# Optimization experiments

Hardware: AMD Instinct MI355X
Metric: run time of the kernel (lower is better)

## Reference

```python
import jax, jax.numpy as jnp
import numpy as np

N, E, H, XD, ED, YD, L = 10000, 640000, 128, 8, 8, 112, 4
EPS_MSG = 1e-7   # GENConv message eps
EPS_SM = 1e-16   # pyg softmax denom eps
EPS_LN = 1e-5    # layernorm eps


def node_ln(x, g, b):
    # torch.nn.LayerNorm over last dim
    m = x.mean(axis=-1, keepdims=True)
    v = x.var(axis=-1, keepdims=True)
    return (x - m) * jax.lax.rsqrt(v + EPS_LN) * g + b


def graph_ln(x, g, b):
    # pyg LayerNorm mode='graph' (no batch): global mean/std over all nodes+channels
    xc = x - x.mean()
    std = jnp.sqrt((xc * xc).mean())
    return xc / (std + EPS_LN) * g + b


def setup_inputs() -> dict:
    key = jax.random.key(0)
    ks = jax.random.split(key, 10)
    rn = lambda k, s, sc: jax.random.normal(k, s, jnp.float32) * sc
    return {
        "x": jax.random.normal(ks[0], (N, XD), jnp.float32),
        "edge_index": jax.random.randint(ks[1], (2, E), 0, N),
        "edge_attr": jax.random.normal(ks[2], (E, ED), jnp.float32),
        "Wn": rn(ks[3], (XD, H), 0.3), "bn": jnp.zeros((H,), jnp.float32),
        "We": rn(ks[4], (ED, H), 0.3), "be": jnp.zeros((H,), jnp.float32),
        "t": jnp.ones((L,), jnp.float32),
        "W1": rn(ks[5], (L, H, 2 * H), 0.08), "b1": jnp.zeros((L, 2 * H), jnp.float32),
        "g1": jnp.ones((L, 2 * H), jnp.float32), "bt1": jnp.zeros((L, 2 * H), jnp.float32),
        "W2": rn(ks[6], (L, 2 * H, H), 0.08), "b2": jnp.zeros((L, H), jnp.float32),
        "lng": jnp.ones((L, H), jnp.float32), "lnb": jnp.zeros((L, H), jnp.float32),
        "Wout": rn(ks[7], (H, YD), 0.08), "bout": jnp.zeros((YD,), jnp.float32),
    }


def reference(x, edge_index, edge_attr, Wn, bn, We, be, t, W1, b1, g1, bt1,
              W2, b2, lng, lnb, Wout, bout):
    src, dst = edge_index[0], edge_index[1]
    h = x @ Wn + bn                       # [N,H] node encoder
    ea = edge_attr @ We + be              # [E,H] edge encoder

    def gen_conv(h, i):
        msg = jax.nn.relu(h[src] + ea) + EPS_MSG          # [E,H]
        logit = msg * t[i]
        mx = jax.ops.segment_max(logit, dst, num_segments=N)
        ex = jnp.exp(logit - mx[dst])
        den = jax.ops.segment_sum(ex, dst, num_segments=N)
        alpha = ex / (den[dst] + EPS_SM)
        agg = jax.ops.segment_sum(alpha * msg, dst, num_segments=N) + h  # root add
        z = jax.nn.relu(graph_ln(agg @ W1[i] + b1[i], g1[i], bt1[i]))
        return z @ W2[i] + b2[i]

    h = gen_conv(h, 0)                    # first layer: conv only
    for i in range(1, L):                 # res+ blocks (dropout off: eval)
        r = jax.nn.relu(node_ln(h, lng[i], lnb[i]))
        h = h + gen_conv(r, i)
    h = jax.nn.relu(node_ln(h, lng[0], lnb[0]))  # layers[0].act(layers[0].norm(x))
    return h @ Wout + bout
```

## Files before the change

### kernel.cpp

```cpp
#include <hip/hip_runtime.h>
#include <math.h>

#define NN 10000
#define NE 640000
#define H 128
#define H2 256
#define XD 8
#define ED 8
#define YD 112
#define NL 4
#define EPS_MSG 1e-7f
#define EPS_SM 1e-16f
#define EPS_LN 1e-5f
#define TM 8
#define NB1 (NN / TM)
#define TNO 16
#define NBO (NN / TNO)

typedef _Float16 h2 __attribute__((ext_vector_type(2)));

__global__ void hist_k(const int* __restrict__ dst, int* __restrict__ counts) {
    int e = blockIdx.x * 256 + threadIdx.x;
    if (e < NE) atomicAdd(&counts[dst[e]], 1);
}

__global__ void scan_k(const int* __restrict__ counts, int* __restrict__ rowptr) {
    __shared__ int part[1024];
    int tid = threadIdx.x;
    const int CH = (NN + 1023) / 1024;
    int base = tid * CH;
    int s = 0;
    for (int j = 0; j < CH; j++) { int i = base + j; if (i < NN) s += counts[i]; }
    part[tid] = s; __syncthreads();
    for (int off = 1; off < 1024; off <<= 1) {
        int v = (tid >= off) ? part[tid - off] : 0;
        __syncthreads();
        part[tid] += v;
        __syncthreads();
    }
    int run = part[tid] - s;
    for (int j = 0; j < CH; j++) {
        int i = base + j;
        if (i < NN) { rowptr[i] = run; run += counts[i]; }
    }
    if (tid == 1023) rowptr[NN] = run;
}

__global__ void scatter_k(const int* __restrict__ dst, const int* __restrict__ rowptr,
                          int* __restrict__ fill, int* __restrict__ perm) {
    int e = blockIdx.x * 256 + threadIdx.x;
    if (e >= NE) return;
    int d = dst[e];
    int pos = rowptr[d] + atomicAdd(&fill[d], 1);
    perm[pos] = e;
}

__global__ void pack_k(const int* __restrict__ perm, const int* __restrict__ src,
                       const float* __restrict__ eattr, int* __restrict__ srcs,
                       _Float16* __restrict__ eacsr) {
    int pos = blockIdx.x * 256 + threadIdx.x;
    if (pos >= NE) return;
    int e = perm[pos];
    srcs[pos] = src[e];
    const float4* ein = (const float4*)eattr;
    float4 a = ein[(size_t)e * 2];
    float4 b = ein[(size_t)e * 2 + 1];
    float4 pack;
    _Float16* pp = (_Float16*)&pack;
    pp[0] = (_Float16)a.x; pp[1] = (_Float16)a.y; pp[2] = (_Float16)a.z; pp[3] = (_Float16)a.w;
    pp[4] = (_Float16)b.x; pp[5] = (_Float16)b.y; pp[6] = (_Float16)b.z; pp[7] = (_Float16)b.w;
    ((float4*)eacsr)[pos] = pack;
}

__global__ void node_enc_k(const float* __restrict__ x, const float* __restrict__ Wn,
                           const float* __restrict__ bn, float* __restrict__ h) {
    int n = blockIdx.x, c = threadIdx.x;
    __shared__ float xl[XD];
    if (c < XD) xl[c] = x[n * XD + c];
    __syncthreads();
    float acc = bn[c];
#pragma unroll
    for (int k = 0; k < XD; k++) acc = fmaf(xl[k], Wn[k * H + c], acc);
    h[(size_t)n * H + c] = acc;
}

__global__ void __launch_bounds__(128) edge_agg_k(
    const float* __restrict__ rin, const int* __restrict__ rowptr,
    const int* __restrict__ srcs, const _Float16* __restrict__ eacsr,
    const float* __restrict__ We, const float* __restrict__ be,
    const float* __restrict__ tptr, int layer, float* __restrict__ agg) {
    int n = blockIdx.x, c = threadIdx.x;
    h2 w01, w23, w45, w67;
    {
        float f0 = We[0 * H + c], f1 = We[1 * H + c], f2 = We[2 * H + c], f3 = We[3 * H + c];
        float f4 = We[4 * H + c], f5 = We[5 * H + c], f6 = We[6 * H + c], f7 = We[7 * H + c];
        w01[0] = (_Float16)f0; w01[1] = (_Float16)f1;
        w23[0] = (_Float16)f2; w23[1] = (_Float16)f3;
        w45[0] = (_Float16)f4; w45[1] = (_Float16)f5;
        w67[0] = (_Float16)f6; w67[1] = (_Float16)f7;
    }
    float bec = be[c];
    float ts2 = tptr[layer] * 1.44269504088896f;
    int beg = rowptr[n], end = rowptr[n + 1];
    float rv = rin[(size_t)n * H + c];
    float den = 0.f, num = 0.f;
#pragma unroll 4
    for (int j = beg; j < end; ++j) {
        int sn = srcs[j];
        float4 raw = *(const float4*)(eacsr + (size_t)j * ED);
        const h2* ep = (const h2*)&raw;
        float hv = rin[(size_t)sn * H + c];
        float p = __builtin_amdgcn_fdot2(ep[0], w01, bec, false);
        p = __builtin_amdgcn_fdot2(ep[1], w23, p, false);
        p = __builtin_amdgcn_fdot2(ep[2], w45, p, false);
        p = __builtin_amdgcn_fdot2(ep[3], w67, p, false);
        float msg = fmaxf(hv + p, 0.f) + EPS_MSG;
        float pe = __builtin_amdgcn_exp2f(msg * ts2);
        den += pe;
        num = fmaf(pe, msg, num);
    }
    agg[(size_t)n * H + c] = num / (den + EPS_SM) + rv;
}

__global__ void __launch_bounds__(256) mm1_k(const float* __restrict__ agg,
    const float* __restrict__ W1i, const float* __restrict__ b1i,
    float* __restrict__ y1, float* __restrict__ part) {
    int nb = blockIdx.x, o = threadIdx.x;
    int n0 = nb * TM;
    __shared__ float a[TM][H];
    for (int t = o; t < TM * H; t += 256) ((float*)a)[t] = agg[(size_t)n0 * H + t];
    __syncthreads();
    float acc[TM];
#pragma unroll
    for (int i = 0; i < TM; i++) acc[i] = 0.f;
    for (int k = 0; k < H; k++) {
        float w = W1i[k * H2 + o];
#pragma unroll
        for (int i = 0; i < TM; i++) acc[i] = fmaf(a[i][k], w, acc[i]);
    }
    float bo = b1i[o];
    float ps = 0.f, ps2 = 0.f;
#pragma unroll
    for (int i = 0; i < TM; i++) {
        float v = acc[i] + bo;
        y1[(size_t)(n0 + i) * H2 + o] = v;
        ps += v; ps2 += v * v;
    }
#pragma unroll
    for (int off = 32; off; off >>= 1) { ps += __shfl_xor(ps, off); ps2 += __shfl_xor(ps2, off); }
    __shared__ float red[8];
    int w = o >> 6;
    if ((o & 63) == 0) { red[w] = ps; red[4 + w] = ps2; }
    __syncthreads();
    if (o == 0) {
        part[nb * 2]     = red[0] + red[1] + red[2] + red[3];
        part[nb * 2 + 1] = red[4] + red[5] + red[6] + red[7];
    }
}

__global__ void __launch_bounds__(256) mm2_k(const float* __restrict__ y1,
    const float* __restrict__ g1i, const float* __restrict__ bt1i,
    const float* __restrict__ W2i, const float* __restrict__ b2i,
    const float* __restrict__ part, float* __restrict__ h,
    const float* __restrict__ lgp, const float* __restrict__ lbp,
    float* __restrict__ r, int first) {
    int nb = blockIdx.x, tid = threadIdx.x;
    int o = tid & 127, half = tid >> 7;
    int rb = half * 4;
    int n0 = nb * TM;
    float s = 0.f, s2 = 0.f;
    for (int i = tid; i < NB1; i += 256) { s += part[2 * i]; s2 += part[2 * i + 1]; }
#pragma unroll
    for (int off = 32; off; off >>= 1) { s += __shfl_xor(s, off); s2 += __shfl_xor(s2, off); }
    __shared__ float sred[8];
    int w4 = tid >> 6;
    if ((tid & 63) == 0) { sred[w4] = s; sred[4 + w4] = s2; }
    __syncthreads();
    const float M = (float)NN * (float)H2;
    float m = (sred[0] + sred[1] + sred[2] + sred[3]) / M;
    float var = fmaxf((sred[4] + sred[5] + sred[6] + sred[7]) / M - m * m, 0.f);
    float istd = 1.f / (sqrtf(var) + EPS_LN);

    __shared__ float z[TM][H2];
    __syncthreads();
    for (int t = tid; t < TM * H2; t += 256) {
        int k = t & 255;
        float v = y1[(size_t)n0 * H2 + t];
        v = (v - m) * istd * g1i[k] + bt1i[k];
        ((float*)z)[t] = fmaxf(v, 0.f);
    }
    __syncthreads();
    float acc[4];
#pragma unroll
    for (int i = 0; i < 4; i++) acc[i] = 0.f;
    for (int k = 0; k < H2; k++) {
        float wv = W2i[k * H + o];
#pragma unroll
        for (int i = 0; i < 4; i++) acc[i] = fmaf(z[rb + i][k], wv, acc[i]);
    }
    float bo = b2i[o];
    float vv[4];
#pragma unroll
    for (int i = 0; i < 4; i++) {
        size_t idx = (size_t)(n0 + rb + i) * H + o;
        float v = acc[i] + bo;
        if (!first) v += h[idx];
        h[idx] = v;
        vv[i] = v;
    }
    __shared__ float rs[2][2][4], rs2[2][2][4];
    int w2 = (tid >> 6) & 1;
#pragma unroll
    for (int i = 0; i < 4; i++) {
        float ss = vv[i], ss2 = vv[i] * vv[i];
#pragma unroll
        for (int off = 32; off; off >>= 1) { ss += __shfl_xor(ss, off); ss2 += __shfl_xor(ss2, off); }
        if ((tid & 63) == 0) { rs[half][w2][i] = ss; rs2[half][w2][i] = ss2; }
    }
    __syncthreads();
    float gc = lgp[o], bc = lbp[o];
#pragma unroll
    for (int i = 0; i < 4; i++) {
        float S = rs[half][0][i] + rs[half][1][i];
        float S2 = rs2[half][0][i] + rs2[half][1][i];
        float mn = S * (1.f / H);
        float vr = S2 * (1.f / H) - mn * mn;
        float inv = rsqrtf(vr + EPS_LN);
        float ov = (vv[i] - mn) * inv * gc + bc;
        r[(size_t)(n0 + rb + i) * H + o] = fmaxf(ov, 0.f);
    }
}

__global__ void __launch_bounds__(128) mmout_k(const float* __restrict__ r,
    const float* __restrict__ Wout, const float* __restrict__ bout,
    float* __restrict__ out) {
    int nb = blockIdx.x, o = threadIdx.x;
    int n0 = nb * TNO;
    __shared__ float a[TNO][H];
    for (int t = o; t < TNO * H; t += 128) ((float*)a)[t] = r[(size_t)n0 * H + t];
    __syncthreads();
    if (o < YD) {
        float acc[TNO];
#pragma unroll
        for (int i = 0; i < TNO; i++) acc[i] = 0.f;
        for (int k = 0; k < H; k++) {
            float w = Wout[k * YD + o];
#pragma unroll
            for (int i = 0; i < TNO; i++) acc[i] = fmaf(a[i][k], w, acc[i]);
        }
        float bo = bout[o];
#pragma unroll
        for (int i = 0; i < TNO; i++) out[(size_t)(n0 + i) * YD + o] = acc[i] + bo;
    }
}

extern "C" void kernel_launch(void* const* d_in, const int* in_sizes, int n_in,
                              void* d_out, int out_size, void* d_ws, size_t ws_size,
                              hipStream_t stream) {
    const float* x    = (const float*)d_in[0];
    const int*   ei   = (const int*)d_in[1];
    const float* eattr= (const float*)d_in[2];
    const float* Wn   = (const float*)d_in[3];
    const float* bn   = (const float*)d_in[4];
    const float* We   = (const float*)d_in[5];
    const float* be   = (const float*)d_in[6];
    const float* t    = (const float*)d_in[7];
    const float* W1   = (const float*)d_in[8];
    const float* b1   = (const float*)d_in[9];
    const float* g1   = (const float*)d_in[10];
    const float* bt1  = (const float*)d_in[11];
    const float* W2   = (const float*)d_in[12];
    const float* b2   = (const float*)d_in[13];
    const float* lng  = (const float*)d_in[14];
    const float* lnb  = (const float*)d_in[15];
    const float* Wout = (const float*)d_in[16];
    const float* bout = (const float*)d_in[17];
    float* out = (float*)d_out;

    const int* src = ei;
    const int* dst = ei + NE;

    char* ws = (char*)d_ws;
    size_t off = 0;
    auto alloc = [&](size_t bytes) -> char* {
        char* p = ws + off;
        off += (bytes + 255) & ~(size_t)255;
        return p;
    };
    int*      counts = (int*)alloc((size_t)NN * 4);
    int*      fill   = (int*)alloc((size_t)NN * 4);
    int*      rowptr = (int*)alloc((size_t)(NN + 1) * 4);
    int*      perm   = (int*)alloc((size_t)NE * 4);
    int*      srcs   = (int*)alloc((size_t)NE * 4);
    _Float16* eacsr  = (_Float16*)alloc((size_t)NE * ED * 2);
    float*    h      = (float*)alloc((size_t)NN * H * 4);
    float*    r      = (float*)alloc((size_t)NN * H * 4);
    float*    agg    = (float*)alloc((size_t)NN * H * 4);
    float*    y1     = (float*)alloc((size_t)NN * H2 * 4);
    float*    part   = (float*)alloc((size_t)NB1 * 2 * 4);
    (void)ws_size; (void)in_sizes; (void)n_in; (void)out_size;

    hipMemsetAsync(counts, 0, (size_t)NN * 4, stream);
    hipMemsetAsync(fill,   0, (size_t)NN * 4, stream);

    hist_k<<<(NE + 255) / 256, 256, 0, stream>>>(dst, counts);
    scan_k<<<1, 1024, 0, stream>>>(counts, rowptr);
    scatter_k<<<(NE + 255) / 256, 256, 0, stream>>>(dst, rowptr, fill, perm);
    pack_k<<<(NE + 255) / 256, 256, 0, stream>>>(perm, src, eattr, srcs, eacsr);
    node_enc_k<<<NN, H, 0, stream>>>(x, Wn, bn, h);

    for (int i = 0; i < NL; i++) {
        const float* cin = (i == 0) ? h : r;
        edge_agg_k<<<NN, H, 0, stream>>>(cin, rowptr, srcs, eacsr, We, be, t, i, agg);
        mm1_k<<<NB1, 256, 0, stream>>>(agg, W1 + (size_t)i * H * H2, b1 + i * H2, y1, part);
        int nx = (i == NL - 1) ? 0 : (i + 1);
        mm2_k<<<NB1, 256, 0, stream>>>(y1, g1 + i * H2, bt1 + i * H2,
                                       W2 + (size_t)i * H2 * H, b2 + i * H, part, h,
                                       lng + nx * H, lnb + nx * H, r, (i == 0) ? 1 : 0);
    }
    mmout_k<<<NBO, 128, 0, stream>>>(r, Wout, bout, out);
}
```

Measured before the change: 489.7 us.

## Use one wavefront per node in edge aggregation and vectorize GEMM loads

The edge aggregation kernel now runs 64 threads per node, each handling two channels, so the per-edge source index and packed edge-attribute loads are shared across two channels per thread. The small dense matmul kernels read activations from LDS as float4 and unroll the k-loop by four, and the LayerNorm/ReLU staging in mm2 moves to float4 loads. The two memsets are merged into one. Halving threads per block in edge_agg_k adds per-thread register use and may reduce latency hiding in the gather loop.

Result: no change. 493.7 us (+0.8%).

```diff
diff --git a/kernel.cpp b/kernel.cpp
--- a/kernel.cpp
+++ b/kernel.cpp
@@ -84,42 +84,51 @@
     h[(size_t)n * H + c] = acc;
 }
 
-__global__ void __launch_bounds__(128) edge_agg_k(
+__global__ void __launch_bounds__(64) edge_agg_k(
     const float* __restrict__ rin, const int* __restrict__ rowptr,
     const int* __restrict__ srcs, const _Float16* __restrict__ eacsr,
     const float* __restrict__ We, const float* __restrict__ be,
     const float* __restrict__ tptr, int layer, float* __restrict__ agg) {
     int n = blockIdx.x, c = threadIdx.x;
-    h2 w01, w23, w45, w67;
-    {
-        float f0 = We[0 * H + c], f1 = We[1 * H + c], f2 = We[2 * H + c], f3 = We[3 * H + c];
-        float f4 = We[4 * H + c], f5 = We[5 * H + c], f6 = We[6 * H + c], f7 = We[7 * H + c];
-        w01[0] = (_Float16)f0; w01[1] = (_Float16)f1;
-        w23[0] = (_Float16)f2; w23[1] = (_Float16)f3;
-        w45[0] = (_Float16)f4; w45[1] = (_Float16)f5;
-        w67[0] = (_Float16)f6; w67[1] = (_Float16)f7;
-    }
-    float bec = be[c];
+    h2 wA[4], wB[4];
+#pragma unroll
+    for (int k = 0; k < 4; k++) {
+        wA[k][0] = (_Float16)We[(2 * k) * H + c];
+        wA[k][1] = (_Float16)We[(2 * k + 1) * H + c];
+        wB[k][0] = (_Float16)We[(2 * k) * H + c + 64];
+        wB[k][1] = (_Float16)We[(2 * k + 1) * H + c + 64];
+    }
+    float becA = be[c], becB = be[c + 64];
     float ts2 = tptr[layer] * 1.44269504088896f;
     int beg = rowptr[n], end = rowptr[n + 1];
-    float rv = rin[(size_t)n * H + c];
-    float den = 0.f, num = 0.f;
+    const float* rn0 = rin + (size_t)n * H + c;
+    float rvA = rn0[0], rvB = rn0[64];
+    float denA = 0.f, numA = 0.f, denB = 0.f, numB = 0.f;
 #pragma unroll 4
     for (int j = beg; j < end; ++j) {
         int sn = srcs[j];
         float4 raw = *(const float4*)(eacsr + (size_t)j * ED);
         const h2* ep = (const h2*)&raw;
-        float hv = rin[(size_t)sn * H + c];
-        float p = __builtin_amdgcn_fdot2(ep[0], w01, bec, false);
-        p = __builtin_amdgcn_fdot2(ep[1], w23, p, false);
-        p = __builtin_amdgcn_fdot2(ep[2], w45, p, false);
-        p = __builtin_amdgcn_fdot2(ep[3], w67, p, false);
-        float msg = fmaxf(hv + p, 0.f) + EPS_MSG;
-        float pe = __builtin_amdgcn_exp2f(msg * ts2);
-        den += pe;
-        num = fmaf(pe, msg, num);
-    }
-    agg[(size_t)n * H + c] = num / (den + EPS_SM) + rv;
+        const float* hp = rin + (size_t)sn * H + c;
+        float hvA = hp[0], hvB = hp[64];
+        float pA = __builtin_amdgcn_fdot2(ep[0], wA[0], becA, false);
+        pA = __builtin_amdgcn_fdot2(ep[1], wA[1], pA, false);
+        pA = __builtin_amdgcn_fdot2(ep[2], wA[2], pA, false);
+        pA = __builtin_amdgcn_fdot2(ep[3], wA[3], pA, false);
+        float pB = __builtin_amdgcn_fdot2(ep[0], wB[0], becB, false);
+        pB = __builtin_amdgcn_fdot2(ep[1], wB[1], pB, false);
+        pB = __builtin_amdgcn_fdot2(ep[2], wB[2], pB, false);
+        pB = __builtin_amdgcn_fdot2(ep[3], wB[3], pB, false);
+        float msgA = fmaxf(hvA + pA, 0.f) + EPS_MSG;
+        float msgB = fmaxf(hvB + pB, 0.f) + EPS_MSG;
+        float peA = __builtin_amdgcn_exp2f(msgA * ts2);
+        float peB = __builtin_amdgcn_exp2f(msgB * ts2);
+        denA += peA; numA = fmaf(peA, msgA, numA);
+        denB += peB; numB = fmaf(peB, msgB, numB);
+    }
+    float* ao = agg + (size_t)n * H + c;
+    ao[0]  = numA / (denA + EPS_SM) + rvA;
+    ao[64] = numB / (denB + EPS_SM) + rvB;
 }
 
 __global__ void __launch_bounds__(256) mm1_k(const float* __restrict__ agg,
@@ -128,15 +137,28 @@
     int nb = blockIdx.x, o = threadIdx.x;
     int n0 = nb * TM;
     __shared__ float a[TM][H];
-    for (int t = o; t < TM * H; t += 256) ((float*)a)[t] = agg[(size_t)n0 * H + t];
+    {
+        const float4* ag4 = (const float4*)(agg + (size_t)n0 * H);
+        float4* a4 = (float4*)a;
+        a4[o] = ag4[o];
+    }
     __syncthreads();
     float acc[TM];
 #pragma unroll
     for (int i = 0; i < TM; i++) acc[i] = 0.f;
-    for (int k = 0; k < H; k++) {
-        float w = W1i[k * H2 + o];
-#pragma unroll
-        for (int i = 0; i < TM; i++) acc[i] = fmaf(a[i][k], w, acc[i]);
+    for (int k = 0; k < H; k += 4) {
+        float w0 = W1i[k * H2 + o];
+        float w1 = W1i[(k + 1) * H2 + o];
+        float w2 = W1i[(k + 2) * H2 + o];
+        float w3 = W1i[(k + 3) * H2 + o];
+#pragma unroll
+        for (int i = 0; i < TM; i++) {
+            float4 av = *(const float4*)&a[i][k];
+            acc[i] = fmaf(av.x, w0, acc[i]);
+            acc[i] = fmaf(av.y, w1, acc[i]);
+            acc[i] = fmaf(av.z, w2, acc[i]);
+            acc[i] = fmaf(av.w, w3, acc[i]);
+        }
     }
     float bo = b1i[o];
     float ps = 0.f, ps2 = 0.f;
@@ -183,20 +205,40 @@
 
     __shared__ float z[TM][H2];
     __syncthreads();
-    for (int t = tid; t < TM * H2; t += 256) {
-        int k = t & 255;
-        float v = y1[(size_t)n0 * H2 + t];
-        v = (v - m) * istd * g1i[k] + bt1i[k];
-        ((float*)z)[t] = fmaxf(v, 0.f);
+    {
+        const float4* y4 = (const float4*)(y1 + (size_t)n0 * H2);
+        const float4* g4 = (const float4*)g1i;
+        const float4* b4 = (const float4*)bt1i;
+        float4* z4 = (float4*)z;
+#pragma unroll
+        for (int t = tid; t < TM * H2 / 4; t += 256) {
+            int k4 = t & 63;
+            float4 v = y4[t];
+            float4 g = g4[k4], b = b4[k4];
+            v.x = fmaxf((v.x - m) * istd * g.x + b.x, 0.f);
+            v.y = fmaxf((v.y - m) * istd * g.y + b.y, 0.f);
+            v.z = fmaxf((v.z - m) * istd * g.z + b.z, 0.f);
+            v.w = fmaxf((v.w - m) * istd * g.w + b.w, 0.f);
+            z4[t] = v;
+        }
     }
     __syncthreads();
     float acc[4];
 #pragma unroll
     for (int i = 0; i < 4; i++) acc[i] = 0.f;
-    for (int k = 0; k < H2; k++) {
-        float wv = W2i[k * H + o];
-#pragma unroll
-        for (int i = 0; i < 4; i++) acc[i] = fmaf(z[rb + i][k], wv, acc[i]);
+    for (int k = 0; k < H2; k += 4) {
+        float w0 = W2i[k * H + o];
+        float w1 = W2i[(k + 1) * H + o];
+        float w2 = W2i[(k + 2) * H + o];
+        float w3 = W2i[(k + 3) * H + o];
+#pragma unroll
+        for (int i = 0; i < 4; i++) {
+            float4 zv = *(const float4*)&z[rb + i][k];
+            acc[i] = fmaf(zv.x, w0, acc[i]);
+            acc[i] = fmaf(zv.y, w1, acc[i]);
+            acc[i] = fmaf(zv.z, w2, acc[i]);
+            acc[i] = fmaf(zv.w, w3, acc[i]);
+        }
     }
     float bo = b2i[o];
     float vv[4];
@@ -209,13 +251,13 @@
         vv[i] = v;
     }
     __shared__ float rs[2][2][4], rs2[2][2][4];
-    int w2 = (tid >> 6) & 1;
+    int w2i_ = (tid >> 6) & 1;
 #pragma unroll
     for (int i = 0; i < 4; i++) {
         float ss = vv[i], ss2 = vv[i] * vv[i];
 #pragma unroll
         for (int off = 32; off; off >>= 1) { ss += __shfl_xor(ss, off); ss2 += __shfl_xor(ss2, off); }
-        if ((tid & 63) == 0) { rs[half][w2][i] = ss; rs2[half][w2][i] = ss2; }
+        if ((tid & 63) == 0) { rs[half][w2i_][i] = ss; rs2[half][w2i_][i] = ss2; }
     }
     __syncthreads();
     float gc = lgp[o], bc = lbp[o];
@@ -237,16 +279,29 @@
     int nb = blockIdx.x, o = threadIdx.x;
     int n0 = nb * TNO;
     __shared__ float a[TNO][H];
-    for (int t = o; t < TNO * H; t += 128) ((float*)a)[t] = r[(size_t)n0 * H + t];
+    {
+        const float4* r4 = (const float4*)(r + (size_t)n0 * H);
+        float4* a4 = (float4*)a;
+        for (int t = o; t < TNO * H / 4; t += 128) a4[t] = r4[t];
+    }
     __syncthreads();
     if (o < YD) {
         float acc[TNO];
 #pragma unroll
         for (int i = 0; i < TNO; i++) acc[i] = 0.f;
-        for (int k = 0; k < H; k++) {
-            float w = Wout[k * YD + o];
-#pragma unroll
-            for (int i = 0; i < TNO; i++) acc[i] = fmaf(a[i][k], w, acc[i]);
+        for (int k = 0; k < H; k += 4) {
+            float w0 = Wout[k * YD + o];
+            float w1 = Wout[(k + 1) * YD + o];
+            float w2 = Wout[(k + 2) * YD + o];
+            float w3 = Wout[(k + 3) * YD + o];
+#pragma unroll
+            for (int i = 0; i < TNO; i++) {
+                float4 av = *(const float4*)&a[i][k];
+                acc[i] = fmaf(av.x, w0, acc[i]);
+                acc[i] = fmaf(av.y, w1, acc[i]);
+                acc[i] = fmaf(av.z, w2, acc[i]);
+                acc[i] = fmaf(av.w, w3, acc[i]);
+            }
         }
         float bo = bout[o];
 #pragma unroll
@@ -287,8 +342,8 @@
         off += (bytes + 255) & ~(size_t)255;
         return p;
     };
-    int*      counts = (int*)alloc((size_t)NN * 4);
-    int*      fill   = (int*)alloc((size_t)NN * 4);
+    int*      counts = (int*)alloc((size_t)NN * 2 * 4);
+    int*      fill   = counts + NN;
     int*      rowptr = (int*)alloc((size_t)(NN + 1) * 4);
     int*      perm   = (int*)alloc((size_t)NE * 4);
     int*      srcs   = (int*)alloc((size_t)NE * 4);
@@ -300,8 +355,7 @@
     float*    part   = (float*)alloc((size_t)NB1 * 2 * 4);
     (void)ws_size; (void)in_sizes; (void)n_in; (void)out_size;
 
-    hipMemsetAsync(counts, 0, (size_t)NN * 4, stream);
-    hipMemsetAsync(fill,   0, (size_t)NN * 4, stream);
+    hipMemsetAsync(counts, 0, (size_t)NN * 2 * 4, stream);
 
     hist_k<<<(NE + 255) / 256, 256, 0, stream>>>(dst, counts);
     scan_k<<<1, 1024, 0, stream>>>(counts, rowptr);
@@ -311,7 +365,7 @@
 
     for (int i = 0; i < NL; i++) {
         const float* cin = (i == 0) ? h : r;
-        edge_agg_k<<<NN, H, 0, stream>>>(cin, rowptr, srcs, eacsr, We, be, t, i, agg);
+        edge_agg_k<<<NN, 64, 0, stream>>>(cin, rowptr, srcs, eacsr, We, be, t, i, agg);
         mm1_k<<<NB1, 256, 0, stream>>>(agg, W1 + (size_t)i * H * H2, b1 + i * H2, y1, part);
         int nx = (i == NL - 1) ? 0 : (i + 1);
         mm2_k<<<NB1, 256, 0, stream>>>(y1, g1 + i * H2, bt1 + i * H2,
```
